# Kernel optimization log

Measured on AMD Instinct MI355X. Metric: run time of the kernel, lower is better.

Reference implementation:

```python
import jax, jax.numpy as jnp
import numpy as np
import math

SCALES = (0.25, 0.125, 0.0625, 0.03125)
CANONICAL_SIZE = 20.0
OUT_SIZE = (5, 5, 5)
SAMPLING_RATIO = 2


def _trilinear(f, pts):
    # f: [C, D0, D1, D2]; pts: [P, 3] in feature-map coords. Returns [C, P].
    Df = jnp.asarray(f.shape[1:], pts.dtype)
    Di = jnp.asarray(f.shape[1:], jnp.int32)
    # ROIAlign convention: samples with any coord < -1 or > D contribute 0.
    valid = jnp.all((pts > -1.0) & (pts < Df), axis=-1)  # [P]
    p = jnp.clip(pts, 0.0, Df - 1.0)
    p0 = jnp.floor(p)
    fr = p - p0                                  # [P,3]
    i0 = p0.astype(jnp.int32)
    i1 = jnp.minimum(i0 + 1, Di - 1)
    w = jnp.stack([1.0 - fr, fr], 0)             # [2,P,3]
    ii = jnp.stack([i0, i1], 0)                  # [2,P,3]
    acc = jnp.zeros((f.shape[0], pts.shape[0]), f.dtype)
    for a in (0, 1):
        for b in (0, 1):
            for c in (0, 1):
                wgt = w[a, :, 0] * w[b, :, 1] * w[c, :, 2]        # [P]
                val = f[:, ii[a, :, 0], ii[b, :, 1], ii[c, :, 2]]  # [C,P]
                acc = acc + val * wgt[None, :]
    return acc * valid[None, :].astype(f.dtype)


def _axis_samples(n, sr):
    # normalized sub-sample centers in (0,1), flattened bin-major: [n*sr]
    bins = jnp.arange(n, dtype=jnp.float32)
    sub = (jnp.arange(sr, dtype=jnp.float32) + 0.5) / sr
    return ((bins[:, None] + sub[None, :]) / n).reshape(-1)


def _pool_one(feats, bidx, roi7, scale):
    # feats: [B,C,D0,D1,D2]; roi7 = [c0,c1,c2,s0,s1,s2,angle_deg]
    f = feats[bidx]                              # [C,D0,D1,D2]
    ctr = roi7[0:3] * scale
    size = roi7[3:6] * scale
    theta = roi7[6] * (math.pi / 180.0)          # pooler op converts deg -> rad
    os0, os1, os2 = OUT_SIZE
    sr = SAMPLING_RATIO
    g0 = (_axis_samples(os0, sr) - 0.5) * size[0]
    g1 = (_axis_samples(os1, sr) - 0.5) * size[1]
    g2 = (_axis_samples(os2, sr) - 0.5) * size[2]
    O0, O1, O2 = jnp.meshgrid(g0, g1, g2, indexing='ij')
    c, s = jnp.cos(theta), jnp.sin(theta)
    # rotation in the (axis0, axis1) plane of the permuted roi coords
    r0 = c * O0 - s * O1
    r1 = s * O0 + c * O1
    pts = jnp.stack([ctr[0] + r0, ctr[1] + r1, ctr[2] + O2], -1)  # [os0*sr,os1*sr,os2*sr,3]
    sampled = _trilinear(f, pts.reshape(-1, 3))                    # [C, P]
    C = f.shape[0]
    sampled = sampled.reshape(C, os0, sr, os1, sr, os2, sr)
    return sampled.mean(axis=(2, 4, 6))          # [C, os0, os1, os2]


def setup_inputs() -> dict:
    key = jax.random.key(0)
    k = jax.random.split(key, 10)
    B, C, R = 2, 64, 128
    x0 = jax.random.normal(k[0], (B, C, 64, 64, 64), jnp.float32)
    x1 = jax.random.normal(k[1], (B, C, 32, 32, 32), jnp.float32)
    x2 = jax.random.normal(k[2], (B, C, 16, 16, 16), jnp.float32)
    x3 = jax.random.normal(k[3], (B, C, 8, 8, 8), jnp.float32)
    ctr = jax.random.uniform(k[4], (R, 3), jnp.float32, 20.0, 236.0)
    dxy = jax.random.uniform(k[5], (R, 2), jnp.float32, 1.0, 16.0)
    dz = jax.random.uniform(k[6], (R, 1), jnp.float32, 1.0, 8.0)
    theta = jax.random.uniform(k[7], (R, 1), jnp.float32, -math.pi, math.pi)
    bbox3d = jnp.concatenate([ctr, dxy, dz, theta], axis=1)  # standard: [x,y,z,dx,dy,dz,theta]
    batch_ids = jax.random.randint(k[8], (R,), 0, B, jnp.int32)
    return {"x0": x0, "x1": x1, "x2": x2, "x3": x3, "bbox3d": bbox3d, "batch_ids": batch_ids}


def reference(x0, x1, x2, x3, bbox3d, batch_ids):
    b = bbox3d
    # convert_to_roi_format: permute [0,2,1,3,5,4,6,7] (drop id col here), angle rad->deg
    roi7 = jnp.stack([b[:, 1], b[:, 0], b[:, 2], b[:, 4], b[:, 3], b[:, 5],
                      b[:, 6] * (180.0 / math.pi)], axis=1)
    # LevelMapper_3d
    size = jnp.sqrt(jnp.maximum(b[:, 3], b[:, 4]))
    rate = size / CANONICAL_SIZE
    levels = jnp.argmin(jnp.abs(jnp.asarray(SCALES, jnp.float32)[None, :] - rate[:, None]), axis=1)
    feats = [x0, x1, x2, x3]
    R, C = roi7.shape[0], x0.shape[1]
    os0, os1, os2 = OUT_SIZE
    result = jnp.zeros((R, C, os0, os1, os2), x0.dtype)
    for l in range(len(SCALES)):
        pooled = jax.vmap(lambda r, bi: _pool_one(feats[l], bi, r, SCALES[l]))(roi7, batch_ids)
        mask = (levels == l)[:, None, None, None, None]
        result = jnp.where(mask, pooled, result)
    return result
```

## Files before the change

### kernel.cpp

```cpp
#include <hip/hip_runtime.h>
#include <math.h>

#define CHB 4
#define C_NUM 64
#define NCELL 125
#define MAX_VOX 256
#define NITEMS 250

__device__ __forceinline__ int swz(int L) { return L ^ ((L >> 3) & 7); }

__device__ __forceinline__ void acc4(const float4* __restrict__ rg4, int v, float w,
                                     float4& A) {
    float4 lo = rg4[swz(v)];
    A.x = fmaf(lo.x, w, A.x); A.y = fmaf(lo.y, w, A.y);
    A.z = fmaf(lo.z, w, A.z); A.w = fmaf(lo.w, w, A.w);
}

__global__ __launch_bounds__(256) void pooler_kernel(
    const float* __restrict__ x0, const float* __restrict__ x1,
    const float* __restrict__ x2, const float* __restrict__ x3,
    const float* __restrict__ bbox, const int* __restrict__ bids,
    float* __restrict__ out)
{
    __shared__ float reg[MAX_VOX * CHB];
    __shared__ float partial[NITEMS * 5];

    const int blk = blockIdx.x;
    const int r   = blk >> 4;
    const int cg  = blk & 15;
    const int tid = threadIdx.x;

    const float b0 = bbox[r*7+0], b1 = bbox[r*7+1], b2 = bbox[r*7+2];
    const float b3 = bbox[r*7+3], b4 = bbox[r*7+4], b5 = bbox[r*7+5];
    const float b6 = bbox[r*7+6];
    const int bid  = bids[r];

    const float rate = sqrtf(fmaxf(b3, b4)) / 20.0f;
    const float SC[4] = {0.25f, 0.125f, 0.0625f, 0.03125f};
    int lvl = 0;
    float best = fabsf(SC[0] - rate);
    #pragma unroll
    for (int j = 1; j < 4; ++j) {
        float d = fabsf(SC[j] - rate);
        if (d < best) { best = d; lvl = j; }
    }
    const float scale = SC[lvl];

    const float* f; int D;
    if (lvl == 0)      { f = x0; D = 64; }
    else if (lvl == 1) { f = x1; D = 32; }
    else if (lvl == 2) { f = x2; D = 16; }
    else               { f = x3; D = 8;  }
    const float Df = (float)D;

    const float ctr0 = b1 * scale;
    const float ctr1 = b0 * scale;
    const float ctr2 = b2 * scale;
    const float sz0  = b4 * scale;
    const float sz1  = b3 * scale;
    const float sz2  = b5 * scale;
    const float theta = (b6 * (180.0f / (float)M_PI)) * ((float)M_PI / 180.0f);
    float st, ct;
    sincosf(theta, &st, &ct);

    const float hx = 0.451f * (fabsf(ct) * sz0 + fabsf(st) * sz1) + 0.01f;
    const float hy = 0.451f * (fabsf(st) * sz0 + fabsf(ct) * sz1) + 0.01f;
    const float hz = 0.451f * sz2 + 0.01f;
    const int x_lo = (int)fminf(fmaxf(ctr0 - hx, 0.0f), Df - 1.0f);
    const int y_lo = (int)fminf(fmaxf(ctr1 - hy, 0.0f), Df - 1.0f);
    const int z_lo = (int)fminf(fmaxf(ctr2 - hz, 0.0f), Df - 1.0f);
    const int x_hi = (int)fminf(fmaxf(ctr0 + hx, 0.0f), Df - 1.0f);
    const int y_hi = (int)fminf(fmaxf(ctr1 + hy, 0.0f), Df - 1.0f);
    const int z_hi = (int)fminf(fmaxf(ctr2 + hz, 0.0f), Df - 1.0f);

    const int nx = min(x_hi - x_lo + 2, D - x_lo);
    const int ny = min(y_hi - y_lo + 2, D - y_lo);
    const int nz = min(z_hi - z_lo + 2, D - z_lo);

    int RX2 = 2; while (RX2 < nx) RX2 <<= 1; RX2 = min(RX2, 8);
    int RY2 = 2; while (RY2 < ny) RY2 <<= 1; RY2 = min(RY2, 8);
    int RZ2 = 2; while (RZ2 < nz) RZ2 <<= 1; RZ2 = min(RZ2, 4);
    const int lz  = __builtin_ctz(RZ2);
    const int ly  = __builtin_ctz(RY2);
    const int sxs = lz + ly;
    const int lnv = __builtin_ctz(RX2) + ly + lz;
    const int nvox = 1 << lnv;

    const size_t vox = (size_t)D * D * D;
    const float* fbase = f + ((size_t)bid * C_NUM + (size_t)cg * CHB) * vox;
    const int total_e = nvox * CHB;
    float vals[4];
    #pragma unroll
    for (int i = 0; i < 4; ++i) {
        int e = tid + (i << 8);
        if (e < total_e) {
            int ch = e >> lnv;
            int v  = e & (nvox - 1);
            int rz = v & (RZ2 - 1);
            int ry = (v >> lz) & (RY2 - 1);
            int rx = v >> sxs;
            int gx = min(x_lo + rx, D - 1);
            int gy = min(y_lo + ry, D - 1);
            int gz = min(z_lo + rz, D - 1);
            vals[i] = fbase[(size_t)ch * vox + (size_t)(gx * D + gy) * D + gz];
        }
    }
    #pragma unroll
    for (int i = 0; i < 4; ++i) {
        int e = tid + (i << 8);
        if (e < total_e) {
            int ch = e >> lnv;
            int v  = e & (nvox - 1);
            reg[swz(v) * 4 + ch] = vals[i];
        }
    }
    __syncthreads();

    if (tid < NITEMS) {
        const int cell  = tid >> 1;
        const int shalf = tid & 1;
        const int i0 = cell / 25;
        const int rem = cell - i0 * 25;
        const int i1 = rem / 5;
        const int i2 = rem - i1 * 5;

        float4 accA = make_float4(0.f, 0.f, 0.f, 0.f);
        const float4* rg4 = (const float4*)reg;

        #pragma unroll
        for (int s = 0; s < 4; ++s) {
            const int s0 = shalf, s1 = (s >> 1) & 1, s2 = s & 1;
            float u0 = ((float)i0 + ((float)s0 + 0.5f) * 0.5f) / 5.0f;
            float u1 = ((float)i1 + ((float)s1 + 0.5f) * 0.5f) / 5.0f;
            float u2 = ((float)i2 + ((float)s2 + 0.5f) * 0.5f) / 5.0f;
            float g0 = (u0 - 0.5f) * sz0;
            float g1 = (u1 - 0.5f) * sz1;
            float g2 = (u2 - 0.5f) * sz2;
            float px = ctr0 + (ct * g0 - st * g1);
            float py = ctr1 + (st * g0 + ct * g1);
            float pz = ctr2 + g2;
            float validf = ((px > -1.0f) && (px < Df) &&
                            (py > -1.0f) && (py < Df) &&
                            (pz > -1.0f) && (pz < Df)) ? 1.0f : 0.0f;
            float q0 = fminf(fmaxf(px, 0.0f), Df - 1.0f);
            float q1 = fminf(fmaxf(py, 0.0f), Df - 1.0f);
            float q2 = fminf(fmaxf(pz, 0.0f), Df - 1.0f);
            int A0 = (int)q0, A1 = (int)q1, A2 = (int)q2;
            float f0 = q0 - (float)A0;
            float f1 = q1 - (float)A1;
            float f2 = q2 - (float)A2;
            int d0 = ((A0 + 1 < D) ? 1 : 0) << sxs;
            int d1 = ((A1 + 1 < D) ? 1 : 0) << lz;
            int d2 = (A2 + 1 < D) ? 1 : 0;
            int base = ((A0 - x_lo) << sxs) + ((A1 - y_lo) << lz) + (A2 - z_lo);

            float wx0 = 1.0f - f0, wx1 = f0;
            float wy0 = 1.0f - f1, wy1 = f1;
            float wz0 = (1.0f - f2) * validf, wz1 = f2 * validf;
            float w00 = wx0 * wy0, w01 = wx0 * wy1;
            float w10 = wx1 * wy0, w11 = wx1 * wy1;

            acc4(rg4, base,                w00 * wz0, accA);
            acc4(rg4, base + d2,           w00 * wz1, accA);
            acc4(rg4, base + d1,           w01 * wz0, accA);
            acc4(rg4, base + d1 + d2,      w01 * wz1, accA);
            acc4(rg4, base + d0,           w10 * wz0, accA);
            acc4(rg4, base + d0 + d2,      w10 * wz1, accA);
            acc4(rg4, base + d0 + d1,      w11 * wz0, accA);
            acc4(rg4, base + d0 + d1 + d2, w11 * wz1, accA);
        }

        const int pb = tid * 5;
        partial[pb + 0] = accA.x; partial[pb + 1] = accA.y;
        partial[pb + 2] = accA.z; partial[pb + 3] = accA.w;
    }
    __syncthreads();

    float4* ob4 = (float4*)(out + (size_t)r * (C_NUM * NCELL) + (size_t)cg * (CHB * NCELL));
    for (int q = tid; q < 125; q += 256) {
        float vres[4];
        #pragma unroll
        for (int j = 0; j < 4; ++j) {
            int o = q * 4 + j;
            unsigned ch = (unsigned)o / 125u;
            int cell = o - (int)ch * 125;
            vres[j] = (partial[(cell * 2) * 5 + ch] +
                       partial[(cell * 2 + 1) * 5 + ch]) * 0.125f;
        }
        ob4[q] = make_float4(vres[0], vres[1], vres[2], vres[3]);
    }
}

extern "C" void kernel_launch(void* const* d_in, const int* in_sizes, int n_in,
                              void* d_out, int out_size, void* d_ws, size_t ws_size,
                              hipStream_t stream) {
    const float* x0   = (const float*)d_in[0];
    const float* x1   = (const float*)d_in[1];
    const float* x2   = (const float*)d_in[2];
    const float* x3   = (const float*)d_in[3];
    const float* bbox = (const float*)d_in[4];
    const int*   bids = (const int*)d_in[5];
    float* out = (float*)d_out;

    hipLaunchKernelGGL(pooler_kernel, dim3(2048), dim3(256), 0, stream,
                       x0, x1, x2, x3, bbox, bids, out);
}
```

Baseline: 188.9 us.

## Process two channel groups per block with both gathers issued up front

Each block now handles two 4-channel groups of one ROI instead of one, which halves the grid to 1024 blocks. It issues the global gathers for both groups before any shared-memory staging, so the second group's load latency overlaps the first group's interpolation. It also amortizes the per-ROI setup (level selection, bounds, sincos) across twice the work. In exchange it doubles shared-memory use per block and leaves fewer blocks to hide latency across the GPU.

```diff
diff --git a/kernel.cpp b/kernel.cpp
--- a/kernel.cpp
+++ b/kernel.cpp
@@ -22,12 +22,13 @@
     const float* __restrict__ bbox, const int* __restrict__ bids,
     float* __restrict__ out)
 {
-    __shared__ float reg[MAX_VOX * CHB];
-    __shared__ float partial[NITEMS * 5];
+    __shared__ float regbuf[2][MAX_VOX * CHB];
+    __shared__ float partial[2][NITEMS * 5];
 
     const int blk = blockIdx.x;
-    const int r   = blk >> 4;
-    const int cg  = blk & 15;
+    const int r      = blk >> 3;
+    const int cgpair = blk & 7;
+    const int cg0    = cgpair * 2;
     const int tid = threadIdx.x;
 
     const float b0 = bbox[r*7+0], b1 = bbox[r*7+1], b2 = bbox[r*7+2];
@@ -85,11 +86,13 @@
     const int sxs = lz + ly;
     const int lnv = __builtin_ctz(RX2) + ly + lz;
     const int nvox = 1 << lnv;
+    const int total_e = nvox * CHB;
 
     const size_t vox = (size_t)D * D * D;
-    const float* fbase = f + ((size_t)bid * C_NUM + (size_t)cg * CHB) * vox;
-    const int total_e = nvox * CHB;
-    float vals[4];
+    const float* fb0 = f + ((size_t)bid * C_NUM + (size_t)cg0 * CHB) * vox;
+    const float* fb1 = fb0 + (size_t)CHB * vox;
+
+    float v0[4], v1[4];
     #pragma unroll
     for (int i = 0; i < 4; ++i) {
         int e = tid + (i << 8);
@@ -99,95 +102,105 @@
             int rz = v & (RZ2 - 1);
             int ry = (v >> lz) & (RY2 - 1);
             int rx = v >> sxs;
-            int gx = min(x_lo + rx, D - 1);
-            int gy = min(y_lo + ry, D - 1);
-            int gz = min(z_lo + rz, D - 1);
-            vals[i] = fbase[(size_t)ch * vox + (size_t)(gx * D + gy) * D + gz];
+            size_t off = (size_t)ch * vox +
+                         (size_t)(min(x_lo + rx, D - 1) * D + min(y_lo + ry, D - 1)) * D +
+                         min(z_lo + rz, D - 1);
+            v0[i] = fb0[off];
+            v1[i] = fb1[off];
         }
     }
+
+    const float4* rg4_0 = (const float4*)regbuf[0];
+    const float4* rg4_1 = (const float4*)regbuf[1];
+
     #pragma unroll
-    for (int i = 0; i < 4; ++i) {
-        int e = tid + (i << 8);
-        if (e < total_e) {
-            int ch = e >> lnv;
-            int v  = e & (nvox - 1);
-            reg[swz(v) * 4 + ch] = vals[i];
-        }
-    }
-    __syncthreads();
-
-    if (tid < NITEMS) {
-        const int cell  = tid >> 1;
-        const int shalf = tid & 1;
-        const int i0 = cell / 25;
-        const int rem = cell - i0 * 25;
-        const int i1 = rem / 5;
-        const int i2 = rem - i1 * 5;
-
-        float4 accA = make_float4(0.f, 0.f, 0.f, 0.f);
-        const float4* rg4 = (const float4*)reg;
-
+    for (int half = 0; half < 2; ++half) {
         #pragma unroll
-        for (int s = 0; s < 4; ++s) {
-            const int s0 = shalf, s1 = (s >> 1) & 1, s2 = s & 1;
-            float u0 = ((float)i0 + ((float)s0 + 0.5f) * 0.5f) / 5.0f;
-            float u1 = ((float)i1 + ((float)s1 + 0.5f) * 0.5f) / 5.0f;
-            float u2 = ((float)i2 + ((float)s2 + 0.5f) * 0.5f) / 5.0f;
-            float g0 = (u0 - 0.5f) * sz0;
-            float g1 = (u1 - 0.5f) * sz1;
-            float g2 = (u2 - 0.5f) * sz2;
-            float px = ctr0 + (ct * g0 - st * g1);
-            float py = ctr1 + (st * g0 + ct * g1);
-            float pz = ctr2 + g2;
-            float validf = ((px > -1.0f) && (px < Df) &&
-                            (py > -1.0f) && (py < Df) &&
-                            (pz > -1.0f) && (pz < Df)) ? 1.0f : 0.0f;
-            float q0 = fminf(fmaxf(px, 0.0f), Df - 1.0f);
-            float q1 = fminf(fmaxf(py, 0.0f), Df - 1.0f);
-            float q2 = fminf(fmaxf(pz, 0.0f), Df - 1.0f);
-            int A0 = (int)q0, A1 = (int)q1, A2 = (int)q2;
-            float f0 = q0 - (float)A0;
-            float f1 = q1 - (float)A1;
-            float f2 = q2 - (float)A2;
-            int d0 = ((A0 + 1 < D) ? 1 : 0) << sxs;
-            int d1 = ((A1 + 1 < D) ? 1 : 0) << lz;
-            int d2 = (A2 + 1 < D) ? 1 : 0;
-            int base = ((A0 - x_lo) << sxs) + ((A1 - y_lo) << lz) + (A2 - z_lo);
-
-            float wx0 = 1.0f - f0, wx1 = f0;
-            float wy0 = 1.0f - f1, wy1 = f1;
-            float wz0 = (1.0f - f2) * validf, wz1 = f2 * validf;
-            float w00 = wx0 * wy0, w01 = wx0 * wy1;
-            float w10 = wx1 * wy0, w11 = wx1 * wy1;
-
-            acc4(rg4, base,                w00 * wz0, accA);
-            acc4(rg4, base + d2,           w00 * wz1, accA);
-            acc4(rg4, base + d1,           w01 * wz0, accA);
-            acc4(rg4, base + d1 + d2,      w01 * wz1, accA);
-            acc4(rg4, base + d0,           w10 * wz0, accA);
-            acc4(rg4, base + d0 + d2,      w10 * wz1, accA);
-            acc4(rg4, base + d0 + d1,      w11 * wz0, accA);
-            acc4(rg4, base + d0 + d1 + d2, w11 * wz1, accA);
-        }
-
-        const int pb = tid * 5;
-        partial[pb + 0] = accA.x; partial[pb + 1] = accA.y;
-        partial[pb + 2] = accA.z; partial[pb + 3] = accA.w;
-    }
-    __syncthreads();
-
-    float4* ob4 = (float4*)(out + (size_t)r * (C_NUM * NCELL) + (size_t)cg * (CHB * NCELL));
-    for (int q = tid; q < 125; q += 256) {
-        float vres[4];
-        #pragma unroll
-        for (int j = 0; j < 4; ++j) {
-            int o = q * 4 + j;
-            unsigned ch = (unsigned)o / 125u;
-            int cell = o - (int)ch * 125;
-            vres[j] = (partial[(cell * 2) * 5 + ch] +
-                       partial[(cell * 2 + 1) * 5 + ch]) * 0.125f;
-        }
-        ob4[q] = make_float4(vres[0], vres[1], vres[2], vres[3]);
+        for (int i = 0; i < 4; ++i) {
+            int e = tid + (i << 8);
+            if (e < total_e) {
+                int ch = e >> lnv;
+                int v  = e & (nvox - 1);
+                regbuf[half][swz(v) * 4 + ch] = half ? v1[i] : v0[i];
+            }
+        }
+        __syncthreads();
+
+        if (tid < NITEMS) {
+            const int cell  = tid >> 1;
+            const int shalf = tid & 1;
+            const int i0 = cell / 25;
+            const int rem = cell - i0 * 25;
+            const int i1 = rem / 5;
+            const int i2 = rem - i1 * 5;
+
+            float4 accA = make_float4(0.f, 0.f, 0.f, 0.f);
+            const float4* rg4 = half ? rg4_1 : rg4_0;
+
+            #pragma unroll
+            for (int s = 0; s < 4; ++s) {
+                const int s0 = shalf, s1 = (s >> 1) & 1, s2 = s & 1;
+                float u0 = ((float)i0 + ((float)s0 + 0.5f) * 0.5f) / 5.0f;
+                float u1 = ((float)i1 + ((float)s1 + 0.5f) * 0.5f) / 5.0f;
+                float u2 = ((float)i2 + ((float)s2 + 0.5f) * 0.5f) / 5.0f;
+                float g0 = (u0 - 0.5f) * sz0;
+                float g1 = (u1 - 0.5f) * sz1;
+                float g2 = (u2 - 0.5f) * sz2;
+                float px = ctr0 + (ct * g0 - st * g1);
+                float py = ctr1 + (st * g0 + ct * g1);
+                float pz = ctr2 + g2;
+                float validf = ((px > -1.0f) && (px < Df) &&
+                                (py > -1.0f) && (py < Df) &&
+                                (pz > -1.0f) && (pz < Df)) ? 1.0f : 0.0f;
+                float q0 = fminf(fmaxf(px, 0.0f), Df - 1.0f);
+                float q1 = fminf(fmaxf(py, 0.0f), Df - 1.0f);
+                float q2 = fminf(fmaxf(pz, 0.0f), Df - 1.0f);
+                int A0 = (int)q0, A1 = (int)q1, A2 = (int)q2;
+                float f0 = q0 - (float)A0;
+                float f1 = q1 - (float)A1;
+                float f2 = q2 - (float)A2;
+                int d0 = ((A0 + 1 < D) ? 1 : 0) << sxs;
+                int d1 = ((A1 + 1 < D) ? 1 : 0) << lz;
+                int d2 = (A2 + 1 < D) ? 1 : 0;
+                int base = ((A0 - x_lo) << sxs) + ((A1 - y_lo) << lz) + (A2 - z_lo);
+
+                float wx0 = 1.0f - f0, wx1 = f0;
+                float wy0 = 1.0f - f1, wy1 = f1;
+                float wz0 = (1.0f - f2) * validf, wz1 = f2 * validf;
+                float w00 = wx0 * wy0, w01 = wx0 * wy1;
+                float w10 = wx1 * wy0, w11 = wx1 * wy1;
+
+                acc4(rg4, base,                w00 * wz0, accA);
+                acc4(rg4, base + d2,           w00 * wz1, accA);
+                acc4(rg4, base + d1,           w01 * wz0, accA);
+                acc4(rg4, base + d1 + d2,      w01 * wz1, accA);
+                acc4(rg4, base + d0,           w10 * wz0, accA);
+                acc4(rg4, base + d0 + d2,      w10 * wz1, accA);
+                acc4(rg4, base + d0 + d1,      w11 * wz0, accA);
+                acc4(rg4, base + d0 + d1 + d2, w11 * wz1, accA);
+            }
+
+            const int pb = tid * 5;
+            partial[half][pb + 0] = accA.x; partial[half][pb + 1] = accA.y;
+            partial[half][pb + 2] = accA.z; partial[half][pb + 3] = accA.w;
+        }
+        __syncthreads();
+
+        float4* ob4 = (float4*)(out + (size_t)r * (C_NUM * NCELL) +
+                                (size_t)(cg0 + half) * (CHB * NCELL));
+        if (tid < 125) {
+            int q = tid;
+            float vres[4];
+            #pragma unroll
+            for (int j = 0; j < 4; ++j) {
+                int o = q * 4 + j;
+                unsigned ch = (unsigned)o / 125u;
+                int cell = o - (int)ch * 125;
+                vres[j] = (partial[half][(cell * 2) * 5 + ch] +
+                           partial[half][(cell * 2 + 1) * 5 + ch]) * 0.125f;
+            }
+            ob4[q] = make_float4(vres[0], vres[1], vres[2], vres[3]);
+        }
     }
 }
 
@@ -202,6 +215,6 @@
     const int*   bids = (const int*)d_in[5];
     float* out = (float*)d_out;
 
-    hipLaunchKernelGGL(pooler_kernel, dim3(2048), dim3(256), 0, stream,
+    hipLaunchKernelGGL(pooler_kernel, dim3(1024), dim3(256), 0, stream,
                        x0, x1, x2, x3, bbox, bids, out);
 }
```

Result: no change. 188.5 us (-0.2%).
